# Kernel optimization log

Measured on AMD Instinct MI355X. Metric: run time of the kernel, lower is better.

Reference implementation:

```python
import jax, jax.numpy as jnp
import numpy as np

K = 0.5  # bottom-k fraction from __init__


def setup_inputs() -> dict:
    key = jax.random.key(0)
    k1, k2 = jax.random.split(key)
    N, V = 8192, 32000
    outputs = jax.random.normal(k1, (N, V), dtype=jnp.float32)
    labels = jax.random.randint(k2, (N,), 0, V, dtype=jnp.int64)
    return {"outputs": outputs, "labels": labels}


def reference(outputs, labels):
    # per-sample cross entropy: logsumexp(logits) - logits[label]
    N = outputs.shape[0]
    logZ = jax.nn.logsumexp(outputs, axis=-1)                             # [N]
    picked = jnp.take_along_axis(outputs, labels[:, None], axis=-1)[:, 0]  # [N]
    ce = logZ - picked                                                     # [N]
    m = int(N * K)  # number of smallest losses kept (K in (0,1])
    # bottom-k via top_k on negated losses (avoids full sort)
    neg_bottom, _ = jax.lax.top_k(-ce, m)
    return jnp.mean(-neg_bottom)
```

## Files before the change

kernel.cpp:

```cpp
#include <hip/hip_runtime.h>
#include <math.h>


#define MAX_N 8192
#define KPT 32

typedef float f32x4 __attribute__((ext_vector_type(4)));

__device__ __forceinline__ unsigned f2k(float f) {
    unsigned u = __float_as_uint(f);
    return (u & 0x80000000u) ? ~u : (u | 0x80000000u);
}
__device__ __forceinline__ float k2f(unsigned k) {
    unsigned u = (k & 0x80000000u) ? (k ^ 0x80000000u) : ~k;
    return __uint_as_float(u);
}

__global__ __launch_bounds__(256) void ce_rows(const float* __restrict__ logits,
                                               const int* __restrict__ labels,
                                               float* __restrict__ ce, int n, int V) {
    const int lane = threadIdx.x & 63;
    const int wid = threadIdx.x >> 6;
    const int row = blockIdx.x * 4 + wid;
    if (row >= n) return;

    const float* rp = logits + (size_t)row * V;
    const f32x4* rp4 = (const f32x4*)rp;
    const int V4 = V >> 2;

    float s0 = 0.f, s1 = 0.f, s2 = 0.f, s3 = 0.f;
    float s4 = 0.f, s5 = 0.f, s6 = 0.f, s7 = 0.f;
    int j = lane;
    for (; j + 64 < V4; j += 128) {
        f32x4 a = rp4[j];
        f32x4 b = rp4[j + 64];
        s0 += __expf(a.x); s1 += __expf(a.y); s2 += __expf(a.z); s3 += __expf(a.w);
        s4 += __expf(b.x); s5 += __expf(b.y); s6 += __expf(b.z); s7 += __expf(b.w);
    }
    for (; j < V4; j += 64) {
        f32x4 a = rp4[j];
        s0 += __expf(a.x); s1 += __expf(a.y); s2 += __expf(a.z); s3 += __expf(a.w);
    }
    for (int t = (V4 << 2) + lane; t < V; t += 64) s0 += __expf(rp[t]);

    float s = ((s0 + s1) + (s2 + s3)) + ((s4 + s5) + (s6 + s7));
    #pragma unroll
    for (int off = 32; off > 0; off >>= 1) s += __shfl_down(s, off, 64);

    if (lane == 0) {
        float picked = rp[labels[row]];
        ce[row] = __logf(s) - picked;
    }
}

__global__ __launch_bounds__(256) void bottomk_mean(const float* __restrict__ ce,
                                                    float* __restrict__ out,
                                                    int n, int m) {
    const int tid = threadIdx.x;
    const int lane = tid & 63, wid = tid >> 6;

    unsigned kreg[KPT];
    #pragma unroll
    for (int p = 0; p < KPT; ++p) {
        int i = tid + p * 256;
        kreg[p] = (i < n) ? f2k(ce[i]) : 0xFFFFFFFFu;
    }

    __shared__ unsigned hist[256];
    __shared__ unsigned scan[256];
    __shared__ unsigned s_prefix, s_remaining;
    if (tid == 0) { s_prefix = 0u; s_remaining = (unsigned)m; }

    unsigned prefmask = 0u;
    for (int shift = 24; shift >= 0; shift -= 8) {
        hist[tid] = 0u;
        __syncthreads();
        const unsigned prefix = s_prefix;
        const unsigned rem = s_remaining;
        #pragma unroll
        for (int p = 0; p < KPT; ++p) {
            unsigned k = kreg[p];
            if ((k & prefmask) == prefix) atomicAdd(&hist[(k >> shift) & 255u], 1u);
        }
        __syncthreads();
        unsigned h = hist[tid];
        scan[tid] = h;
        __syncthreads();
        #pragma unroll
        for (int off = 1; off < 256; off <<= 1) {
            unsigned t = (tid >= off) ? scan[tid - off] : 0u;
            __syncthreads();
            scan[tid] += t;
            __syncthreads();
        }
        unsigned incl = scan[tid];
        unsigned excl = incl - h;
        if (excl < rem && incl >= rem) {
            s_prefix = prefix | ((unsigned)tid << shift);
            s_remaining = rem - excl;
        }
        prefmask |= (255u << shift);
        __syncthreads();
    }

    const unsigned T = s_prefix;
    float lsum = 0.f;
    unsigned lcnt = 0u;
    #pragma unroll
    for (int p = 0; p < KPT; ++p) {
        unsigned k = kreg[p];
        if (k < T) { lsum += k2f(k); lcnt++; }
    }
    #pragma unroll
    for (int off = 32; off > 0; off >>= 1) {
        lsum += __shfl_down(lsum, off, 64);
        lcnt += __shfl_down(lcnt, off, 64);
    }
    __shared__ float wsum[4];
    __shared__ unsigned wcnt[4];
    if (lane == 0) { wsum[wid] = lsum; wcnt[wid] = lcnt; }
    __syncthreads();
    if (tid == 0) {
        float tot = (wsum[0] + wsum[1]) + (wsum[2] + wsum[3]);
        unsigned cnt = (wcnt[0] + wcnt[1]) + (wcnt[2] + wcnt[3]);
        tot += (float)((unsigned)m - cnt) * k2f(T);
        out[0] = tot / (float)m;
    }
}

extern "C" void kernel_launch(void* const* d_in, const int* in_sizes, int n_in,
                              void* d_out, int out_size, void* d_ws, size_t ws_size,
                              hipStream_t stream) {
    const float* logits = (const float*)d_in[0];
    const int* labels = (const int*)d_in[1];
    float* out = (float*)d_out;
    float* ce = (float*)d_ws;

    const int N = in_sizes[1];
    const int V = in_sizes[0] / N;
    const int M = N / 2;

    const int rows_per_block = 4;
    ce_rows<<<(N + rows_per_block - 1) / rows_per_block, 256, 0, stream>>>(logits, labels, ce, N, V);
    bottomk_mean<<<1, 256, 0, stream>>>(ce, out, N, M);
}
```

Baseline: 211.7 us.

## Software-pipeline row loads in CE kernel and use wave-shuffle scan in bottom-k

The logsumexp loop now processes 256-vector blocks with a three-stage register pipeline, issuing loads two blocks ahead so memory latency overlaps the exp work. The label-gathered logit is loaded at kernel start instead of after the reduction. The bottom-k radix select replaces its shared-memory Hillis-Steele scan, which had many barriers, with a wave-level shuffle scan plus a 4-entry cross-wave combine. The pipeline uses more registers, which may lower occupancy.

```diff
diff --git a/kernel.cpp b/kernel.cpp
--- a/kernel.cpp
+++ b/kernel.cpp
@@ -28,17 +28,45 @@
     const f32x4* rp4 = (const f32x4*)rp;
     const int V4 = V >> 2;
 
+    const float picked = rp[labels[row]];
+
+    const int B = 256;
+    const int nb = V4 / B;
+
     float s0 = 0.f, s1 = 0.f, s2 = 0.f, s3 = 0.f;
     float s4 = 0.f, s5 = 0.f, s6 = 0.f, s7 = 0.f;
-    int j = lane;
-    for (; j + 64 < V4; j += 128) {
-        f32x4 a = rp4[j];
-        f32x4 b = rp4[j + 64];
-        s0 += __expf(a.x); s1 += __expf(a.y); s2 += __expf(a.z); s3 += __expf(a.w);
-        s4 += __expf(b.x); s5 += __expf(b.y); s6 += __expf(b.z); s7 += __expf(b.w);
+
+#define CONSUME(a, b, c, d)                                                       \
+    do {                                                                          \
+        s0 += __expf((a).x); s1 += __expf((a).y); s2 += __expf((a).z); s3 += __expf((a).w); \
+        s4 += __expf((b).x); s5 += __expf((b).y); s6 += __expf((b).z); s7 += __expf((b).w); \
+        s0 += __expf((c).x); s1 += __expf((c).y); s2 += __expf((c).z); s3 += __expf((c).w); \
+        s4 += __expf((d).x); s5 += __expf((d).y); s6 += __expf((d).z); s7 += __expf((d).w); \
+    } while (0)
+
+    if (nb >= 2) {
+        f32x4 p0 = rp4[lane],       p1 = rp4[lane + 64];
+        f32x4 p2 = rp4[lane + 128], p3 = rp4[lane + 192];
+        int jq = B + lane;
+        f32x4 q0 = rp4[jq], q1 = rp4[jq + 64], q2 = rp4[jq + 128], q3 = rp4[jq + 192];
+        for (int b = 2; b < nb; ++b) {
+            const int jr = b * B + lane;
+            f32x4 r0 = rp4[jr], r1 = rp4[jr + 64], r2 = rp4[jr + 128], r3 = rp4[jr + 192];
+            CONSUME(p0, p1, p2, p3);
+            p0 = q0; p1 = q1; p2 = q2; p3 = q3;
+            q0 = r0; q1 = r1; q2 = r2; q3 = r3;
+        }
+        CONSUME(p0, p1, p2, p3);
+        CONSUME(q0, q1, q2, q3);
+    } else if (nb == 1) {
+        f32x4 p0 = rp4[lane],       p1 = rp4[lane + 64];
+        f32x4 p2 = rp4[lane + 128], p3 = rp4[lane + 192];
+        CONSUME(p0, p1, p2, p3);
     }
-    for (; j < V4; j += 64) {
-        f32x4 a = rp4[j];
+#undef CONSUME
+
+    for (int t = nb * B + lane; t < V4; t += 64) {
+        f32x4 a = rp4[t];
         s0 += __expf(a.x); s1 += __expf(a.y); s2 += __expf(a.z); s3 += __expf(a.w);
     }
     for (int t = (V4 << 2) + lane; t < V; t += 64) s0 += __expf(rp[t]);
@@ -47,10 +75,7 @@
     #pragma unroll
     for (int off = 32; off > 0; off >>= 1) s += __shfl_down(s, off, 64);
 
-    if (lane == 0) {
-        float picked = rp[labels[row]];
-        ce[row] = __logf(s) - picked;
-    }
+    if (lane == 0) ce[row] = __logf(s) - picked;
 }
 
 __global__ __launch_bounds__(256) void bottomk_mean(const float* __restrict__ ce,
@@ -67,7 +92,7 @@
     }
 
     __shared__ unsigned hist[256];
-    __shared__ unsigned scan[256];
+    __shared__ unsigned wtot[4];
     __shared__ unsigned s_prefix, s_remaining;
     if (tid == 0) { s_prefix = 0u; s_remaining = (unsigned)m; }
 
@@ -83,18 +108,20 @@
             if ((k & prefmask) == prefix) atomicAdd(&hist[(k >> shift) & 255u], 1u);
         }
         __syncthreads();
-        unsigned h = hist[tid];
-        scan[tid] = h;
+        const unsigned h = hist[tid];
+        unsigned x = h;
+        #pragma unroll
+        for (int off = 1; off < 64; off <<= 1) {
+            unsigned t = __shfl_up(x, off, 64);
+            if (lane >= off) x += t;
+        }
+        if (lane == 63) wtot[wid] = x;
         __syncthreads();
+        unsigned wo = 0;
         #pragma unroll
-        for (int off = 1; off < 256; off <<= 1) {
-            unsigned t = (tid >= off) ? scan[tid - off] : 0u;
-            __syncthreads();
-            scan[tid] += t;
-            __syncthreads();
-        }
-        unsigned incl = scan[tid];
-        unsigned excl = incl - h;
+        for (int w = 0; w < 4; ++w) wo += (w < wid) ? wtot[w] : 0u;
+        const unsigned incl = x + wo;
+        const unsigned excl = incl - h;
         if (excl < rem && incl >= rem) {
             s_prefix = prefix | ((unsigned)tid << shift);
             s_remaining = rem - excl;
```

Result: faster. 203.5 us (-3.9%).
